# Kernel optimization log

Hardware: AMD Instinct MI355X
Metric: run time of the kernel (lower is better)

The kernel has to match this reference:

```python
import jax, jax.numpy as jnp
import numpy as np
from jax import lax

T = 16        # in_length
E = 32        # input_embedding_size_d
H = 64        # encoder_size
NG = 32       # vehicles per scene group
G = 1024      # number of scene groups
N = G * NG    # total vehicles
C = 3         # class_num

leaky = lambda x: jax.nn.leaky_relu(x, 0.1)

def _gru_final(x_seq, Wih, Whh, bih, bhh):
    # x_seq: (T, N, E). PyTorch GRU gate order: r, z, n. Returns final hidden (N, H).
    def step(h, x):
        gx = x @ Wih.T + bih
        gh = h @ Whh.T + bhh
        xr, xz, xn = jnp.split(gx, 3, axis=-1)
        hr, hz, hn = jnp.split(gh, 3, axis=-1)
        r = jax.nn.sigmoid(xr + hr)
        z = jax.nn.sigmoid(xz + hz)
        ng = jnp.tanh(xn + r * hn)
        return (1.0 - z) * ng + z * h, None
    h0 = jnp.zeros((x_seq.shape[1], Whh.shape[1]), x_seq.dtype)
    hT, _ = lax.scan(step, h0, x_seq)
    return hT

def setup_inputs() -> dict:
    key = jax.random.key(0)
    ks = jax.random.split(key, 24)
    def rn(k, shape, fan):
        return jax.random.normal(k, shape, jnp.float32) * np.float32(1.0 / np.sqrt(fan))
    inp = {}
    inp["scene"] = jax.random.normal(ks[0], (N, 2 * T), jnp.float32)
    inp["condition"] = jax.random.randint(ks[1], (N,), 0, C, jnp.int32)
    inp["hero_pos_index"] = jax.random.randint(ks[2], (G,), 0, N, jnp.int32)
    inp["nbrs_pos_index"] = jax.random.randint(ks[3], (N,), 0, N, jnp.int32)
    inp["index_div"] = jnp.arange(N, dtype=jnp.int32).reshape(G, NG)
    # ip_emb_d: Linear(2, E)
    inp["W_emb"] = rn(ks[4], (2, E), 2)
    inp["b_emb"] = jnp.zeros((E,), jnp.float32)
    # forward / backward GRUs (weight_ih: (3H,E), weight_hh: (3H,H))
    inp["Wih_f"] = rn(ks[5], (3 * H, E), E); inp["Whh_f"] = rn(ks[6], (3 * H, H), H)
    inp["bih_f"] = jnp.zeros((3 * H,), jnp.float32); inp["bhh_f"] = jnp.zeros((3 * H,), jnp.float32)
    inp["Wih_b"] = rn(ks[7], (3 * H, E), E); inp["Whh_b"] = rn(ks[8], (3 * H, H), H)
    inp["bih_b"] = jnp.zeros((3 * H,), jnp.float32); inp["bhh_b"] = jnp.zeros((3 * H,), jnp.float32)
    # mlp: Linear(H, H//2)
    inp["Wm"] = rn(ks[9], (H, H // 2), H); inp["bm"] = jnp.zeros((H // 2,), jnp.float32)
    # spatial_mlp: Linear(2T, H) -> Linear(H, H//2)
    inp["Ws1"] = rn(ks[10], (2 * T, H), 2 * T); inp["bs1"] = jnp.zeros((H,), jnp.float32)
    inp["Ws2"] = rn(ks[11], (H, H // 2), H); inp["bs2"] = jnp.zeros((H // 2,), jnp.float32)
    # op_d: Linear(H, H//4) -> Linear(H//4, C)
    inp["Wo1"] = rn(ks[12], (H, H // 4), H); inp["bo1"] = jnp.zeros((H // 4,), jnp.float32)
    inp["Wo2"] = rn(ks[13], (H // 4, C), H // 4); inp["bo2"] = jnp.zeros((C,), jnp.float32)
    return inp

def reference(scene, condition, hero_pos_index, nbrs_pos_index, index_div,
              W_emb, b_emb, Wih_f, Whh_f, bih_f, bhh_f, Wih_b, Whh_b, bih_b, bhh_b,
              Wm, bm, Ws1, bs1, Ws2, bs2, Wo1, bo1, Wo2, bo2):
    n_total = scene.shape[0]
    # scene.view(-1,2,T).permute(2,0,1) -> (T, N, 2)
    scene_t = scene.reshape(n_total, 2, T).transpose(2, 0, 1)
    emb = leaky(scene_t @ W_emb + b_emb)                 # (T, N, E)
    h_f = _gru_final(emb, Wih_f, Whh_f, bih_f, bhh_f)    # (N, H)
    h_b = _gru_final(emb[::-1], Wih_b, Whh_b, bih_b, bhh_b)
    seq_enc = leaky(((h_f + h_b) * 0.5) @ Wm + bm)       # (N, H//2)
    # pairwise relative features within each group: rel[g, j, i] = x_i - x_j
    feat_g = scene[index_div]                            # (G, n, 2T); row layout == permute(1,2,0).view(-1,2T)
    rel = feat_g[:, None, :, :] - feat_g[:, :, None, :]  # (G, n, n, 2T)
    enc = leaky(leaky(rel @ Ws1 + bs1) @ Ws2 + bs2)      # (G, n, n, H//2)
    # diagonal pairs (i==j) are dropped in the original; subtract mlp(0) then divide by n-1
    zero_enc = leaky(leaky(bs1) @ Ws2 + bs2)             # (H//2,)
    n_grp = index_div.shape[1]
    pooled = (enc.sum(axis=2) - zero_enc) / (n_grp - 1)  # (G, n, H//2)
    pooled = pooled.reshape(n_total, -1)                 # group-concat order == vehicle order (arange groups)
    full_enc = jnp.concatenate([seq_enc, pooled], axis=1)  # (N, H)
    x_logit = leaky(full_enc @ Wo1 + bo1) @ Wo2 + bo2      # (N, C)
    return x_logit, full_enc
```

## Files before the change

### kernel.cpp

```cpp
#include <hip/hip_runtime.h>
#include <hip/hip_bf16.h>

#define TT 16
#define EE 32
#define HH 64
#define NGRP 32
#define CC 3

typedef __attribute__((ext_vector_type(8))) short short8;
typedef __attribute__((ext_vector_type(4))) float floatx4;

#define MFMA16(a, b, c) __builtin_amdgcn_mfma_f32_16x16x32_bf16((a), (b), (c), 0, 0, 0)

#define RLN2 1.4426950408889634f

__device__ __forceinline__ float leakyf(float x) { return fmaxf(x, 0.1f * x); }
__device__ __forceinline__ short f2bf(float x) {
    unsigned u = __float_as_uint(x);
    return (short)((u + 0x7FFFu + ((u >> 16) & 1u)) >> 16);
}
__device__ __forceinline__ short f2bf_h(float x) {
    return (short)((__float_as_uint(x) + 0x8000u) >> 16);
}
__device__ __forceinline__ float bf2f(short s) {
    return __uint_as_float(((unsigned)(unsigned short)s) << 16);
}
__device__ __forceinline__ short8 ld8bf(const float* __restrict__ p) {
    const float4 a = *(const float4*)p;
    const float4 b = *(const float4*)(p + 4);
    short8 v;
    v[0] = f2bf(a.x); v[1] = f2bf(a.y); v[2] = f2bf(a.z); v[3] = f2bf(a.w);
    v[4] = f2bf(b.x); v[5] = f2bf(b.y); v[6] = f2bf(b.z); v[7] = f2bf(b.w);
    return v;
}
__device__ __forceinline__ short8 ld8bfs(const float* __restrict__ p, float s) {
    const float4 a = *(const float4*)p;
    const float4 b = *(const float4*)(p + 4);
    short8 v;
    v[0] = f2bf(a.x * s); v[1] = f2bf(a.y * s); v[2] = f2bf(a.z * s); v[3] = f2bf(a.w * s);
    v[4] = f2bf(b.x * s); v[5] = f2bf(b.y * s); v[6] = f2bf(b.z * s); v[7] = f2bf(b.w * s);
    return v;
}

__global__ __launch_bounds__(512, 4) void fused_kernel(
    const float* __restrict__ scene, const int* __restrict__ index_div,
    const float* __restrict__ W_emb, const float* __restrict__ b_emb,
    const float* __restrict__ Wih_f, const float* __restrict__ Whh_f,
    const float* __restrict__ bih_f, const float* __restrict__ bhh_f,
    const float* __restrict__ Wih_b, const float* __restrict__ Whh_b,
    const float* __restrict__ bih_b, const float* __restrict__ bhh_b,
    const float* __restrict__ Wm, const float* __restrict__ bm,
    const float* __restrict__ Ws1, const float* __restrict__ bs1,
    const float* __restrict__ Ws2, const float* __restrict__ bs2,
    const float* __restrict__ Wo1, const float* __restrict__ bo1,
    const float* __restrict__ Wo2, const float* __restrict__ bo2,
    float* __restrict__ full_enc, float* __restrict__ out)
{
    __shared__ float sscene[32][33];
    __shared__ __align__(16) union SmemU {
        struct {
            short Xall[16 * 2 * 64 * 8];
            short Hf[2 * 2 * 2 * 2 * 64 * 8];
        } g;
        struct {
            float su[NGRP][68];
            float fe[NGRP][68];
            float swo1[1024];
            float szero[32];
        } s;
    } sm;

    const int g    = blockIdx.x;
    const int tid  = threadIdx.x;
    const int lane = tid & 63;
    const int w    = __builtin_amdgcn_readfirstlane(tid >> 6);
    const int dir  = w >> 2;
    const int wd   = w & 3;
    const int cc   = lane & 15;
    const int quad = lane >> 4;
    const int j    = wd * 16 + cc;
    const int ks_w = j >> 5;
    const int qa_w = (j >> 3) & 3;
    const int ii_w = j & 7;
    const int rlane = (lane & 48) | ((lane & 3) << 2) | ((lane >> 2) & 3);

    #pragma unroll
    for (int rep = 0; rep < 2; ++rep) {
        const int idx = tid + rep * 512;
        const int v = idx >> 5, c = idx & 31;
        const int n = index_div[g * NGRP + v];
        sscene[c][v] = scene[n * 32 + c];
    }

    const float* Wih = dir ? Wih_b : Wih_f;
    const float* Whh = dir ? Whh_b : Whh_f;
    const float* bih = dir ? bih_b : bih_f;
    const float* bhh = dir ? bhh_b : bhh_f;
    const int k0 = quad * 8;
    const float SRZ = -RLN2, SN = 2.0f * RLN2;
    const short8 Br0  = ld8bfs(Whh + (j      ) * 64 + k0,      SRZ);
    const short8 Br1  = ld8bfs(Whh + (j      ) * 64 + 32 + k0, SRZ);
    const short8 Br2  = ld8bfs(Wih + (j      ) * 32 + k0,      SRZ);
    const short8 Bz0  = ld8bfs(Whh + (j +  64) * 64 + k0,      SRZ);
    const short8 Bz1  = ld8bfs(Whh + (j +  64) * 64 + 32 + k0, SRZ);
    const short8 Bz2  = ld8bfs(Wih + (j +  64) * 32 + k0,      SRZ);
    const short8 Bhn0 = ld8bfs(Whh + (j + 128) * 64 + k0,      SN);
    const short8 Bhn1 = ld8bfs(Whh + (j + 128) * 64 + 32 + k0, SN);
    const short8 Bxn  = ld8bfs(Wih + (j + 128) * 32 + k0,      SN);
    const float vb_r  = SRZ * (bih[j] + bhh[j]);
    const float vb_z  = SRZ * (bih[j + 64] + bhh[j + 64]);
    const float vb_xn = SN * bih[j + 128];
    const float vb_hn = SN * bhh[j + 128];

    __syncthreads();

    {
        const int t   = tid >> 5;
        const int veh = tid & 31;
        const float xs = sscene[t][veh];
        const float ys = sscene[16 + t][veh];
        const int mt = veh >> 4;
        const int m  = veh & 15;
        #pragma unroll
        for (int q = 0; q < 4; ++q) {
            short8 v;
            #pragma unroll
            for (int i2 = 0; i2 < 8; ++i2) {
                const int e = q * 8 + i2;
                v[i2] = f2bf(leakyf(fmaf(xs, W_emb[e], fmaf(ys, W_emb[EE + e], b_emb[e]))));
            }
            *(short8*)&sm.g.Xall[(((t * 2 + mt) * 64) + q * 16 + m) * 8] = v;
        }
        const short8 z8 = {0, 0, 0, 0, 0, 0, 0, 0};
        *(short8*)&sm.g.Hf[(tid >> 8) * 4096 + (tid & 255) * 8] = z8;
    }

    float h_reg[8];
    #pragma unroll
    for (int i = 0; i < 8; ++i) h_reg[i] = 0.0f;

    const int hf_dir = dir * 4096;
    __syncthreads();

    #pragma unroll 2
    for (int s = 0; s < TT; ++s) {
        const int pb = s & 1, nb = pb ^ 1;
        const int t  = dir ? (TT - 1 - s) : s;
        const short* HfD = &sm.g.Hf[hf_dir + pb * 2048];
        short*       HfN = &sm.g.Hf[hf_dir + nb * 2048];
        #pragma unroll
        for (int mt = 0; mt < 2; ++mt) {
            const short8 Ah0 = *(const short8*)&HfD[((0 * 2 + mt) * 64 + rlane) * 8];
            const short8 Ah1 = *(const short8*)&HfD[((1 * 2 + mt) * 64 + rlane) * 8];
            const short8 Axx = *(const short8*)&sm.g.Xall[((t * 2 + mt) * 64 + lane) * 8];
            const floatx4 z4 = {0.f, 0.f, 0.f, 0.f};
            const floatx4 ar  = MFMA16(Axx, Br2, MFMA16(Ah1, Br1, MFMA16(Ah0, Br0, z4)));
            const floatx4 az  = MFMA16(Axx, Bz2, MFMA16(Ah1, Bz1, MFMA16(Ah0, Bz0, z4)));
            const floatx4 ahn = MFMA16(Ah1, Bhn1, MFMA16(Ah0, Bhn0, z4));
            const floatx4 axn = MFMA16(Axx, Bxn, z4);
            #pragma unroll
            for (int r = 0; r < 4; ++r) {
                const float rr = __builtin_amdgcn_rcpf(1.0f + __builtin_amdgcn_exp2f(ar[r] + vb_r));
                const float zz = __builtin_amdgcn_rcpf(1.0f + __builtin_amdgcn_exp2f(az[r] + vb_z));
                const float y  = fmaf(rr, ahn[r] + vb_hn, axn[r] + vb_xn);
                const float ng = fmaf(-2.0f,
                                      __builtin_amdgcn_rcpf(__builtin_amdgcn_exp2f(y) + 1.0f),
                                      1.0f);
                const float h0 = h_reg[mt * 4 + r];
                h_reg[mt * 4 + r] = fmaf(zz, h0 - ng, ng);
            }
        }
        #pragma unroll
        for (int mt = 0; mt < 2; ++mt) {
            #pragma unroll
            for (int r = 0; r < 4; ++r) {
                const int slot = qa_w * 16 + r * 4 + quad;
                HfN[((ks_w * 2 + mt) * 64 + slot) * 8 + ii_w] = f2bf_h(h_reg[mt * 4 + r]);
            }
        }
        __syncthreads();
    }

    if (w < 4) {
        const int nt   = w >> 1;
        const int mt_e = w & 1;
        const int n_col = nt * 16 + cc;
        short8 Bm0, Bm1;
        #pragma unroll
        for (int i = 0; i < 8; ++i) {
            Bm0[i] = f2bf(Wm[(     quad * 8 + i) * 32 + n_col]);
            Bm1[i] = f2bf(Wm[(32 + quad * 8 + i) * 32 + n_col]);
        }
        short8 A0, A1;
        #pragma unroll
        for (int ks = 0; ks < 2; ++ks) {
            const short8 F = *(const short8*)&sm.g.Hf[0    + ((ks * 2 + mt_e) * 64 + rlane) * 8];
            const short8 B = *(const short8*)&sm.g.Hf[4096 + ((ks * 2 + mt_e) * 64 + rlane) * 8];
            #pragma unroll
            for (int i = 0; i < 8; ++i) {
                const short v = f2bf(0.5f * (bf2f(F[i]) + bf2f(B[i])));
                if (ks == 0) A0[i] = v; else A1[i] = v;
            }
        }
        const floatx4 z4 = {0.f, 0.f, 0.f, 0.f};
        const floatx4 acc = MFMA16(A1, Bm1, MFMA16(A0, Bm0, z4));
        const float bmn = bm[n_col];
        #pragma unroll
        for (int r = 0; r < 4; ++r) {
            const int veh = mt_e * 16 + quad * 4 + r;
            const float sv = leakyf(acc[r] + bmn);
            const int n = index_div[g * NGRP + veh];
            full_enc[n * HH + n_col] = sv;
            sm.s.fe[veh][n_col] = sv;
        }
    } else {
        const int l  = tid & 255;
        const int v  = l >> 3;
        const int d0 = (l & 7) * 8;
        float acc[8];
        #pragma unroll
        for (int i = 0; i < 8; ++i) acc[i] = 0.0f;
        #pragma unroll
        for (int e = 0; e < EE; ++e) {
            const float f = sscene[e][v];
            const float4 w0 = *(const float4*)&Ws1[e * 64 + d0];
            const float4 w1 = *(const float4*)&Ws1[e * 64 + d0 + 4];
            acc[0] = fmaf(f, w0.x, acc[0]); acc[1] = fmaf(f, w0.y, acc[1]);
            acc[2] = fmaf(f, w0.z, acc[2]); acc[3] = fmaf(f, w0.w, acc[3]);
            acc[4] = fmaf(f, w1.x, acc[4]); acc[5] = fmaf(f, w1.y, acc[5]);
            acc[6] = fmaf(f, w1.z, acc[6]); acc[7] = fmaf(f, w1.w, acc[7]);
        }
        #pragma unroll
        for (int i = 0; i < 8; ++i) sm.s.su[v][d0 + i] = acc[i];
        *(float4*)&sm.s.swo1[l * 4] = *(const float4*)&Wo1[l * 4];
        if (l < 32) {
            float zs = bs2[l];
            #pragma unroll
            for (int d = 0; d < HH; ++d) zs = fmaf(leakyf(bs1[d]), Ws2[d * 32 + l], zs);
            sm.s.szero[l] = leakyf(zs);
        }
    }

    short8 Bw00, Bw01, Bw10, Bw11;
    #pragma unroll
    for (int i = 0; i < 8; ++i) {
        Bw00[i] = f2bf(Ws2[(     quad * 8 + i) * 32 + cc]);
        Bw01[i] = f2bf(Ws2[(32 + quad * 8 + i) * 32 + cc]);
        Bw10[i] = f2bf(Ws2[(     quad * 8 + i) * 32 + 16 + cc]);
        Bw11[i] = f2bf(Ws2[(32 + quad * 8 + i) * 32 + 16 + cc]);
    }
    float bsq0[8], bsq1[8];
    #pragma unroll
    for (int i = 0; i < 8; ++i) {
        bsq0[i] = bs1[quad * 8 + i];
        bsq1[i] = bs1[32 + quad * 8 + i];
    }
    const float bs2c0 = bs2[cc], bs2c1 = bs2[16 + cc];
    __syncthreads();

    #pragma unroll 2
    for (int jj = 0; jj < 4; ++jj) {
        const int jrow = w * 4 + jj;
        float vj0[8], vj1[8];
        #pragma unroll
        for (int i = 0; i < 8; ++i) {
            vj0[i] = sm.s.su[jrow][quad * 8 + i] - bsq0[i];
            vj1[i] = sm.s.su[jrow][32 + quad * 8 + i] - bsq1[i];
        }
        float acc0 = 0.0f, acc1 = 0.0f;
        #pragma unroll
        for (int it = 0; it < 2; ++it) {
            const int irow = it * 16 + cc;
            const float4 p0 = *(const float4*)&sm.s.su[irow][quad * 8];
            const float4 p1 = *(const float4*)&sm.s.su[irow][quad * 8 + 4];
            const float4 p2 = *(const float4*)&sm.s.su[irow][32 + quad * 8];
            const float4 p3 = *(const float4*)&sm.s.su[irow][32 + quad * 8 + 4];
            short8 A0, A1;
            A0[0] = f2bf(leakyf(p0.x - vj0[0])); A0[1] = f2bf(leakyf(p0.y - vj0[1]));
            A0[2] = f2bf(leakyf(p0.z - vj0[2])); A0[3] = f2bf(leakyf(p0.w - vj0[3]));
            A0[4] = f2bf(leakyf(p1.x - vj0[4])); A0[5] = f2bf(leakyf(p1.y - vj0[5]));
            A0[6] = f2bf(leakyf(p1.z - vj0[6])); A0[7] = f2bf(leakyf(p1.w - vj0[7]));
            A1[0] = f2bf(leakyf(p2.x - vj1[0])); A1[1] = f2bf(leakyf(p2.y - vj1[1]));
            A1[2] = f2bf(leakyf(p2.z - vj1[2])); A1[3] = f2bf(leakyf(p2.w - vj1[3]));
            A1[4] = f2bf(leakyf(p3.x - vj1[4])); A1[5] = f2bf(leakyf(p3.y - vj1[5]));
            A1[6] = f2bf(leakyf(p3.z - vj1[6])); A1[7] = f2bf(leakyf(p3.w - vj1[7]));
            const floatx4 z4 = {0.f, 0.f, 0.f, 0.f};
            const floatx4 D0 = MFMA16(A1, Bw01, MFMA16(A0, Bw00, z4));
            const floatx4 D1 = MFMA16(A1, Bw11, MFMA16(A0, Bw10, z4));
            #pragma unroll
            for (int r = 0; r < 4; ++r) {
                acc0 += leakyf(D0[r] + bs2c0);
                acc1 += leakyf(D1[r] + bs2c1);
            }
        }
        acc0 += __shfl_xor(acc0, 16, 64); acc0 += __shfl_xor(acc0, 32, 64);
        acc1 += __shfl_xor(acc1, 16, 64); acc1 += __shfl_xor(acc1, 32, 64);
        const int n = index_div[g * NGRP + jrow];
        if (quad == 0) {
            const float pv = (acc0 - sm.s.szero[cc]) * (1.0f / 31.0f);
            full_enc[n * HH + 32 + cc] = pv;
            sm.s.fe[jrow][32 + cc] = pv;
        } else if (quad == 1) {
            const float pv = (acc1 - sm.s.szero[16 + cc]) * (1.0f / 31.0f);
            full_enc[n * HH + 48 + cc] = pv;
            sm.s.fe[jrow][48 + cc] = pv;
        }
    }
    __syncthreads();

    {
        const int veh = tid >> 4;
        const int p   = tid & 15;
        float a = bo1[p];
        #pragma unroll
        for (int k = 0; k < HH; ++k)
            a = fmaf(sm.s.fe[veh][k], sm.s.swo1[k * 16 + p], a);
        a = leakyf(a);
        float l0 = a * Wo2[p * 3 + 0];
        float l1 = a * Wo2[p * 3 + 1];
        float l2 = a * Wo2[p * 3 + 2];
        #pragma unroll
        for (int off = 1; off < 16; off <<= 1) {
            l0 += __shfl_xor(l0, off, 64);
            l1 += __shfl_xor(l1, off, 64);
            l2 += __shfl_xor(l2, off, 64);
        }
        if (p == 0) {
            const int n = index_div[g * NGRP + veh];
            out[n * 3 + 0] = l0 + bo2[0];
            out[n * 3 + 1] = l1 + bo2[1];
            out[n * 3 + 2] = l2 + bo2[2];
        }
    }
}

extern "C" void kernel_launch(void* const* d_in, const int* in_sizes, int n_in,
                              void* d_out, int out_size, void* d_ws, size_t ws_size,
                              hipStream_t stream) {
    const float* scene     = (const float*)d_in[0];
    const int*   index_div = (const int*)d_in[4];
    const float* W_emb = (const float*)d_in[5];
    const float* b_emb = (const float*)d_in[6];
    const float* Wih_f = (const float*)d_in[7];
    const float* Whh_f = (const float*)d_in[8];
    const float* bih_f = (const float*)d_in[9];
    const float* bhh_f = (const float*)d_in[10];
    const float* Wih_b = (const float*)d_in[11];
    const float* Whh_b = (const float*)d_in[12];
    const float* bih_b = (const float*)d_in[13];
    const float* bhh_b = (const float*)d_in[14];
    const float* Wm  = (const float*)d_in[15];
    const float* bm  = (const float*)d_in[16];
    const float* Ws1 = (const float*)d_in[17];
    const float* bs1 = (const float*)d_in[18];
    const float* Ws2 = (const float*)d_in[19];
    const float* bs2 = (const float*)d_in[20];
    const float* Wo1 = (const float*)d_in[21];
    const float* bo1 = (const float*)d_in[22];
    const float* Wo2 = (const float*)d_in[23];
    const float* bo2 = (const float*)d_in[24];

    const int N = in_sizes[0] / (2 * TT);
    const int G = in_sizes[4] / NGRP;

    float* out      = (float*)d_out;
    float* full_enc = out + (size_t)N * CC;

    fused_kernel<<<dim3(G), dim3(512), 0, stream>>>(
        scene, index_div, W_emb, b_emb, Wih_f, Whh_f, bih_f, bhh_f,
        Wih_b, Whh_b, bih_b, bhh_b, Wm, bm, Ws1, bs1, Ws2, bs2,
        Wo1, bo1, Wo2, bo2, full_enc, out);
}
```

Baseline: 191.3 us.

## Shrink LDS footprint by single-buffering GRU hidden state and aliasing scene tile

The hidden-state buffer for the recurrence goes from double- to single-buffered, with an extra barrier each step between the reads and the writes. The scene staging tile now aliases the Hf region during embedding and is reloaded from global memory into the post-loop union struct. Launch bounds are raised to request more resident blocks. The aim is to cut per-block LDS so more blocks fit per CU and the grid runs in fewer waves. The cost is an extra barrier per timestep, a second gather of the scene data, and possible register spilling under the tighter launch bound.

Result: slower. 453.0 us (+136.8%).

```diff
diff --git a/kernel.cpp b/kernel.cpp
--- a/kernel.cpp
+++ b/kernel.cpp
@@ -42,7 +42,7 @@
     return v;
 }
 
-__global__ __launch_bounds__(512, 4) void fused_kernel(
+__global__ __launch_bounds__(512, 8) void fused_kernel(
     const float* __restrict__ scene, const int* __restrict__ index_div,
     const float* __restrict__ W_emb, const float* __restrict__ b_emb,
     const float* __restrict__ Wih_f, const float* __restrict__ Whh_f,
@@ -56,17 +56,17 @@
     const float* __restrict__ Wo2, const float* __restrict__ bo2,
     float* __restrict__ full_enc, float* __restrict__ out)
 {
-    __shared__ float sscene[32][33];
     __shared__ __align__(16) union SmemU {
         struct {
             short Xall[16 * 2 * 64 * 8];
-            short Hf[2 * 2 * 2 * 2 * 64 * 8];
+            short Hf[2 * 2 * 2 * 64 * 8];
         } g;
         struct {
             float su[NGRP][68];
             float fe[NGRP][68];
             float swo1[1024];
             float szero[32];
+            float sscene2[32][33];
         } s;
     } sm;
 
@@ -84,12 +84,15 @@
     const int ii_w = j & 7;
     const int rlane = (lane & 48) | ((lane & 3) << 2) | ((lane >> 2) & 3);
 
-    #pragma unroll
-    for (int rep = 0; rep < 2; ++rep) {
-        const int idx = tid + rep * 512;
-        const int v = idx >> 5, c = idx & 31;
-        const int n = index_div[g * NGRP + v];
-        sscene[c][v] = scene[n * 32 + c];
+    {
+        float* sc0 = (float*)sm.g.Hf;
+        #pragma unroll
+        for (int rep = 0; rep < 2; ++rep) {
+            const int idx = tid + rep * 512;
+            const int v = idx >> 5, c = idx & 31;
+            const int n = index_div[g * NGRP + v];
+            sc0[c * 33 + v] = scene[n * 32 + c];
+        }
     }
 
     const float* Wih = dir ? Wih_b : Wih_f;
@@ -115,10 +118,11 @@
     __syncthreads();
 
     {
+        const float* sc0 = (const float*)sm.g.Hf;
         const int t   = tid >> 5;
         const int veh = tid & 31;
-        const float xs = sscene[t][veh];
-        const float ys = sscene[16 + t][veh];
+        const float xs = sc0[t * 33 + veh];
+        const float ys = sc0[(16 + t) * 33 + veh];
         const int mt = veh >> 4;
         const int m  = veh & 15;
         #pragma unroll
@@ -131,23 +135,24 @@
             }
             *(short8*)&sm.g.Xall[(((t * 2 + mt) * 64) + q * 16 + m) * 8] = v;
         }
+    }
+    __syncthreads();
+    {
         const short8 z8 = {0, 0, 0, 0, 0, 0, 0, 0};
-        *(short8*)&sm.g.Hf[(tid >> 8) * 4096 + (tid & 255) * 8] = z8;
+        *(short8*)&sm.g.Hf[tid * 8] = z8;
     }
 
     float h_reg[8];
     #pragma unroll
     for (int i = 0; i < 8; ++i) h_reg[i] = 0.0f;
 
-    const int hf_dir = dir * 4096;
+    const int hf_dir = dir * 2048;
     __syncthreads();
 
     #pragma unroll 2
     for (int s = 0; s < TT; ++s) {
-        const int pb = s & 1, nb = pb ^ 1;
         const int t  = dir ? (TT - 1 - s) : s;
-        const short* HfD = &sm.g.Hf[hf_dir + pb * 2048];
-        short*       HfN = &sm.g.Hf[hf_dir + nb * 2048];
+        const short* HfD = &sm.g.Hf[hf_dir];
         #pragma unroll
         for (int mt = 0; mt < 2; ++mt) {
             const short8 Ah0 = *(const short8*)&HfD[((0 * 2 + mt) * 64 + rlane) * 8];
@@ -170,16 +175,27 @@
                 h_reg[mt * 4 + r] = fmaf(zz, h0 - ng, ng);
             }
         }
+        __syncthreads();
+        short* HfW = &sm.g.Hf[hf_dir];
         #pragma unroll
         for (int mt = 0; mt < 2; ++mt) {
             #pragma unroll
             for (int r = 0; r < 4; ++r) {
                 const int slot = qa_w * 16 + r * 4 + quad;
-                HfN[((ks_w * 2 + mt) * 64 + slot) * 8 + ii_w] = f2bf_h(h_reg[mt * 4 + r]);
+                HfW[((ks_w * 2 + mt) * 64 + slot) * 8 + ii_w] = f2bf_h(h_reg[mt * 4 + r]);
             }
         }
         __syncthreads();
     }
+
+    #pragma unroll
+    for (int rep = 0; rep < 2; ++rep) {
+        const int idx = tid + rep * 512;
+        const int v = idx >> 5, c = idx & 31;
+        const int n = index_div[g * NGRP + v];
+        sm.s.sscene2[c][v] = scene[n * 32 + c];
+    }
+    __syncthreads();
 
     if (w < 4) {
         const int nt   = w >> 1;
@@ -195,7 +211,7 @@
         #pragma unroll
         for (int ks = 0; ks < 2; ++ks) {
             const short8 F = *(const short8*)&sm.g.Hf[0    + ((ks * 2 + mt_e) * 64 + rlane) * 8];
-            const short8 B = *(const short8*)&sm.g.Hf[4096 + ((ks * 2 + mt_e) * 64 + rlane) * 8];
+            const short8 B = *(const short8*)&sm.g.Hf[2048 + ((ks * 2 + mt_e) * 64 + rlane) * 8];
             #pragma unroll
             for (int i = 0; i < 8; ++i) {
                 const short v = f2bf(0.5f * (bf2f(F[i]) + bf2f(B[i])));
@@ -222,7 +238,7 @@
         for (int i = 0; i < 8; ++i) acc[i] = 0.0f;
         #pragma unroll
         for (int e = 0; e < EE; ++e) {
-            const float f = sscene[e][v];
+            const float f = sm.s.sscene2[e][v];
             const float4 w0 = *(const float4*)&Ws1[e * 64 + d0];
             const float4 w1 = *(const float4*)&Ws1[e * 64 + d0 + 4];
             acc[0] = fmaf(f, w0.x, acc[0]); acc[1] = fmaf(f, w0.y, acc[1]);
```
